# Performance work log

Measured on AMD Instinct MI355X. Metric: run time of the kernel, lower is better.

The kernel has to match this reference:

```python
import jax, jax.numpy as jnp
import numpy as np

KERNEL_SIZE = 4
STRIDE = 4


def setup_inputs() -> dict:
    key = jax.random.key(0)
    ks = jax.random.split(key, 5)
    b, l, d, hidden = 32, 8192, 256, 512
    x = jax.random.normal(ks[0], (b, l, d), dtype=jnp.float32)
    We = jax.random.normal(ks[1], (d, hidden), dtype=jnp.float32) * (1.0 / np.sqrt(d))
    be = jax.random.normal(ks[2], (hidden,), dtype=jnp.float32) * 0.01
    Wr = jax.random.normal(ks[3], (hidden, 1), dtype=jnp.float32) * (1.0 / np.sqrt(hidden))
    br = jax.random.normal(ks[4], (1,), dtype=jnp.float32) * 0.01
    return {"x": x, "We": We, "be": be, "Wr": Wr, "br": br}


def reference(x, We, be, Wr, br):
    b, l, d = x.shape
    steps = (l - KERNEL_SIZE) // STRIDE + 1
    # window gather: original loop slices x[:, i*stride : i*stride+stride, :]
    idx = jnp.arange(steps)[:, None] * STRIDE + jnp.arange(STRIDE)[None, :]  # (steps, stride)
    win = x[:, idx, :]  # (b, steps, stride, d)
    h = jnp.tanh(win @ We + be)                      # (b, steps, stride, hidden)
    logits = jnp.squeeze(h @ Wr, -1) + br            # (b, steps, stride)
    w = jax.nn.softmax(jax.nn.sigmoid(logits), axis=-1)
    out = jnp.einsum('bswd,bsw->bsd', win, w)        # softmax-weighted sum over window
    return out
```

## Files before the change

### kernel.cpp

```cpp
#include <hip/hip_runtime.h>
#include <hip/hip_bf16.h>

typedef __attribute__((ext_vector_type(8))) short bf16x8;
typedef __attribute__((ext_vector_type(4))) float f32x4;

#define D        256
#define NH       512
#define NT       32
#define KT       8
#define MT       4
#define ROWS_PER_BLOCK 64
#define ROWS_TOTAL (32*8192)
#define BFRAG    131072

typedef __attribute__((address_space(1))) const void GV;
typedef __attribute__((address_space(3))) void LV;

__device__ __forceinline__ short f2bf(float f) {
    union { float f; unsigned u; } v; v.f = f;
    unsigned r = v.u + 0x7FFFu + ((v.u >> 16) & 1u);
    return (short)(r >> 16);
}
__device__ __forceinline__ float rcp_fast(float x) {
    return __builtin_amdgcn_rcpf(x);
}

__global__ void prepack_B(const float* __restrict__ We, const float* __restrict__ be,
                          const float* __restrict__ Wr,
                          short* __restrict__ Bh, float2* __restrict__ bw,
                          float* __restrict__ Ssum, int ncopy) {
    int i = blockIdx.x * 256 + threadIdx.x;
    int k = i >> 9;
    int n = i & 511;
    int nt = n >> 4, c = n & 15;
    int kt = k >> 5, g = (k >> 3) & 3, j = k & 7;
    int idx = (((nt * 8 + kt) * 64) + (g * 16 + c)) * 8 + j;
    short v = f2bf(We[i]);
    for (int cp = 0; cp < ncopy; ++cp)
        Bh[cp * BFRAG + idx] = v;
    if (i < 512) bw[i] = make_float2(2.0f * be[i], Wr[i]);
    if (i == 0) {
        float s = 0.0f;
        for (int t = 0; t < 512; ++t) s += Wr[t];
        Ssum[0] = s;
    }
}

__global__ __launch_bounds__(64, 2) void softpool_main(
    const float* __restrict__ x, const short* __restrict__ Bh,
    const float2* __restrict__ bwg, const float* __restrict__ br,
    const float* __restrict__ Ssum, float* __restrict__ out, int cmask)
{
    const int lane = threadIdx.x;
    const int c = lane & 15;
    const int g = lane >> 4;
    const long row0 = (long)blockIdx.x * ROWS_PER_BLOCK;

    __shared__ short Bl[2][4096];
    __shared__ float2 bwl[512];

    const short* gB = Bh + (long)(blockIdx.x & cmask) * BFRAG + lane * 8;

    #define STAGE(buf, ntv) {                                                  \
        const short* _g = gB + (long)(ntv) * 4096;                             \
        _Pragma("unroll")                                                      \
        for (int kk = 0; kk < 8; ++kk)                                         \
            __builtin_amdgcn_global_load_lds((GV*)(_g + kk * 512),             \
                (LV*)&Bl[buf][kk * 512], 16, 0, 0);                            \
    }

    #define VM0 asm volatile("s_waitcnt vmcnt(0)" ::: "memory");

    STAGE(0, 0)

    #pragma unroll
    for (int i = 0; i < 4; ++i) {
        float4 v = ((const float4*)bwg)[lane * 4 + i];
        ((float4*)bwl)[lane * 4 + i] = v;
    }

    bf16x8 a[MT][KT];
    #pragma unroll
    for (int m = 0; m < MT; ++m) {
        const float* xr = x + (row0 + m * 16 + c) * D + g * 8;
        #pragma unroll
        for (int kt = 0; kt < KT; ++kt) {
            float4 v0 = *(const float4*)(xr + kt * 32);
            float4 v1 = *(const float4*)(xr + kt * 32 + 4);
            bf16x8 t;
            t[0] = f2bf(v0.x); t[1] = f2bf(v0.y); t[2] = f2bf(v0.z); t[3] = f2bf(v0.w);
            t[4] = f2bf(v1.x); t[5] = f2bf(v1.y); t[6] = f2bf(v1.z); t[7] = f2bf(v1.w);
            a[m][kt] = t;
        }
    }

    float lps[MT][4];
    #pragma unroll
    for (int m = 0; m < MT; ++m)
        #pragma unroll
        for (int r = 0; r < 4; ++r) lps[m][r] = 0.0f;

    f32x4 accA[MT], accB[MT];

    #define MFMA_(buf, accv) {                                                 \
        _Pragma("unroll")                                                      \
        for (int m = 0; m < MT; ++m)                                           \
            _Pragma("unroll")                                                  \
            for (int r = 0; r < 4; ++r) accv[m][r] = 0.0f;                     \
        _Pragma("unroll")                                                      \
        for (int kt = 0; kt < KT; ++kt) {                                      \
            bf16x8 b = *(const bf16x8*)&Bl[buf][kt * 512 + lane * 8];          \
            _Pragma("unroll")                                                  \
            for (int m = 0; m < MT; ++m)                                       \
                accv[m] = __builtin_amdgcn_mfma_f32_16x16x32_bf16(             \
                             a[m][kt], b, accv[m], 0, 0, 0);                   \
        }                                                                      \
    }

    #define TANH_(accv, ntv) {                                                 \
        float2 bwv = bwl[(ntv) * 16 + c];                                      \
        _Pragma("unroll")                                                      \
        for (int m = 0; m < MT; ++m)                                           \
            _Pragma("unroll")                                                  \
            for (int r = 0; r < 4; ++r) {                                      \
                float z = __builtin_fmaf(accv[m][r], 2.0f, bwv.x);             \
                float e = __expf(z);                                           \
                float rr = rcp_fast(e + 1.0f);                                 \
                lps[m][r] = __builtin_fmaf(bwv.y, rr, lps[m][r]);              \
            }                                                                  \
    }

    VM0
    STAGE(1, 1)
    MFMA_(0, accA)
    VM0

    for (int it = 0; it < 15; ++it) {
        STAGE(0, 2 * it + 2)
        MFMA_(1, accB)
        TANH_(accA, 2 * it)
        VM0
        STAGE(1, 2 * it + 3)
        MFMA_(0, accA)
        TANH_(accB, 2 * it + 1)
        VM0
    }
    MFMA_(1, accB)
    TANH_(accA, 30)
    TANH_(accB, 31)

    const float brv = br[0];
    const float S = Ssum[0];
    #pragma unroll
    for (int m = 0; m < MT; ++m) {
        float l0 = lps[m][0], l1 = lps[m][1], l2 = lps[m][2], l3 = lps[m][3];
        #pragma unroll
        for (int off = 1; off < 16; off <<= 1) {
            l0 += __shfl_xor(l0, off, 64);
            l1 += __shfl_xor(l1, off, 64);
            l2 += __shfl_xor(l2, off, 64);
            l3 += __shfl_xor(l3, off, 64);
        }
        float g0 = S - 2.0f * l0 + brv;
        float g1 = S - 2.0f * l1 + brv;
        float g2 = S - 2.0f * l2 + brv;
        float g3 = S - 2.0f * l3 + brv;
        float s0 = rcp_fast(1.0f + __expf(-g0));
        float s1 = rcp_fast(1.0f + __expf(-g1));
        float s2 = rcp_fast(1.0f + __expf(-g2));
        float s3 = rcp_fast(1.0f + __expf(-g3));
        float e0 = __expf(s0), e1 = __expf(s1), e2 = __expf(s2), e3 = __expf(s3);
        float inv = rcp_fast(e0 + e1 + e2 + e3);
        float w0 = e0 * inv, w1 = e1 * inv, w2 = e2 * inv, w3 = e3 * inv;

        const long wrow = row0 + m * 16 + g * 4;
        const long W = wrow >> 2;
        const float* xw = x + wrow * D + c * 4;
        float* op = out + W * D + c * 4;
        #pragma unroll
        for (int q = 0; q < 4; ++q) {
            float4 r0 = *(const float4*)(xw + 0 * D + q * 64);
            float4 r1 = *(const float4*)(xw + 1 * D + q * 64);
            float4 r2 = *(const float4*)(xw + 2 * D + q * 64);
            float4 r3 = *(const float4*)(xw + 3 * D + q * 64);
            float4 oo;
            oo.x = w0 * r0.x + w1 * r1.x + w2 * r2.x + w3 * r3.x;
            oo.y = w0 * r0.y + w1 * r1.y + w2 * r2.y + w3 * r3.y;
            oo.z = w0 * r0.z + w1 * r1.z + w2 * r2.z + w3 * r3.z;
            oo.w = w0 * r0.w + w1 * r1.w + w2 * r2.w + w3 * r3.w;
            *(float4*)(op + q * 64) = oo;
        }
    }
}

extern "C" void kernel_launch(void* const* d_in, const int* in_sizes, int n_in,
                              void* d_out, int out_size, void* d_ws, size_t ws_size,
                              hipStream_t stream) {
    const float* x  = (const float*)d_in[0];
    const float* We = (const float*)d_in[1];
    const float* be = (const float*)d_in[2];
    const float* Wr = (const float*)d_in[3];
    const float* br = (const float*)d_in[4];
    float* out = (float*)d_out;

    const int ncopy = (ws_size >= (size_t)8 * BFRAG * 2 + 8192) ? 8 : 1;

    char* ws = (char*)d_ws;
    short*  Bh   = (short*)ws;
    float2* bwp  = (float2*)(ws + (size_t)ncopy * BFRAG * 2);
    float*  Ssum = (float*)((char*)bwp + 4096);

    prepack_B<<<BFRAG / 256, 256, 0, stream>>>(We, be, Wr, Bh, bwp, Ssum, ncopy);

    const int blocks = ROWS_TOTAL / ROWS_PER_BLOCK;
    softpool_main<<<blocks, 64, 0, stream>>>(x, Bh, bwp, br, Ssum, out, ncopy - 1);
}
```

Measured before the change: 163.1 us.

## Load x rows coalesced and transpose through swizzled LDS; drop B replicas

The A-operand load now reads whole x rows with fully coalesced float4 loads, converts them to bf16, writes them into LDS with an XOR swizzle, and reads the MFMA fragments back from LDS. This replaces the earlier strided per-lane gathers. The LDS used is buffer 0 of the B double buffer, so B staging now starts in buffer 1 and the ping-pong order is swapped. The multiple replicated copies of the packed B weights are removed, so every block reads one shared copy. This shrinks the prepack work but may increase L2 contention on that single copy.

```diff
diff --git a/kernel.cpp b/kernel.cpp
--- a/kernel.cpp
+++ b/kernel.cpp
@@ -2,6 +2,7 @@
 #include <hip/hip_bf16.h>
 
 typedef __attribute__((ext_vector_type(8))) short bf16x8;
+typedef __attribute__((ext_vector_type(4))) short short4v;
 typedef __attribute__((ext_vector_type(4))) float f32x4;
 
 #define D        256
@@ -11,7 +12,6 @@
 #define MT       4
 #define ROWS_PER_BLOCK 64
 #define ROWS_TOTAL (32*8192)
-#define BFRAG    131072
 
 typedef __attribute__((address_space(1))) const void GV;
 typedef __attribute__((address_space(3))) void LV;
@@ -28,16 +28,14 @@
 __global__ void prepack_B(const float* __restrict__ We, const float* __restrict__ be,
                           const float* __restrict__ Wr,
                           short* __restrict__ Bh, float2* __restrict__ bw,
-                          float* __restrict__ Ssum, int ncopy) {
+                          float* __restrict__ Ssum) {
     int i = blockIdx.x * 256 + threadIdx.x;
     int k = i >> 9;
     int n = i & 511;
     int nt = n >> 4, c = n & 15;
     int kt = k >> 5, g = (k >> 3) & 3, j = k & 7;
     int idx = (((nt * 8 + kt) * 64) + (g * 16 + c)) * 8 + j;
-    short v = f2bf(We[i]);
-    for (int cp = 0; cp < ncopy; ++cp)
-        Bh[cp * BFRAG + idx] = v;
+    Bh[idx] = f2bf(We[i]);
     if (i < 512) bw[i] = make_float2(2.0f * be[i], Wr[i]);
     if (i == 0) {
         float s = 0.0f;
@@ -49,7 +47,7 @@
 __global__ __launch_bounds__(64, 2) void softpool_main(
     const float* __restrict__ x, const short* __restrict__ Bh,
     const float2* __restrict__ bwg, const float* __restrict__ br,
-    const float* __restrict__ Ssum, float* __restrict__ out, int cmask)
+    const float* __restrict__ Ssum, float* __restrict__ out)
 {
     const int lane = threadIdx.x;
     const int c = lane & 15;
@@ -59,7 +57,7 @@
     __shared__ short Bl[2][4096];
     __shared__ float2 bwl[512];
 
-    const short* gB = Bh + (long)(blockIdx.x & cmask) * BFRAG + lane * 8;
+    const short* gB = Bh + lane * 8;
 
     #define STAGE(buf, ntv) {                                                  \
         const short* _g = gB + (long)(ntv) * 4096;                             \
@@ -71,7 +69,7 @@
 
     #define VM0 asm volatile("s_waitcnt vmcnt(0)" ::: "memory");
 
-    STAGE(0, 0)
+    STAGE(1, 0)
 
     #pragma unroll
     for (int i = 0; i < 4; ++i) {
@@ -80,17 +78,30 @@
     }
 
     bf16x8 a[MT][KT];
+    char* Asl = (char*)&Bl[0][0];
     #pragma unroll
     for (int m = 0; m < MT; ++m) {
-        const float* xr = x + (row0 + m * 16 + c) * D + g * 8;
+        #pragma unroll
+        for (int half = 0; half < 2; ++half) {
+            const float* rb = x + (row0 + m * 16 + half * 8) * D;
+            float4 st[8];
+            #pragma unroll
+            for (int i = 0; i < 8; ++i)
+                st[i] = ((const float4*)(rb + i * D))[lane];
+            #pragma unroll
+            for (int i = 0; i < 8; ++i) {
+                const int row = half * 8 + i;
+                short4v t;
+                t[0] = f2bf(st[i].x); t[1] = f2bf(st[i].y);
+                t[2] = f2bf(st[i].z); t[3] = f2bf(st[i].w);
+                const int boff = row * 512 + ((lane * 8) ^ ((row & 7) << 4));
+                *(short4v*)(Asl + boff) = t;
+            }
+        }
         #pragma unroll
         for (int kt = 0; kt < KT; ++kt) {
-            float4 v0 = *(const float4*)(xr + kt * 32);
-            float4 v1 = *(const float4*)(xr + kt * 32 + 4);
-            bf16x8 t;
-            t[0] = f2bf(v0.x); t[1] = f2bf(v0.y); t[2] = f2bf(v0.z); t[3] = f2bf(v0.w);
-            t[4] = f2bf(v1.x); t[5] = f2bf(v1.y); t[6] = f2bf(v1.z); t[7] = f2bf(v1.w);
-            a[m][kt] = t;
+            const int boff = c * 512 + ((kt * 64 + g * 16) ^ ((c & 7) << 4));
+            a[m][kt] = *(const bf16x8*)(Asl + boff);
         }
     }
 
@@ -131,21 +142,21 @@
     }
 
     VM0
-    STAGE(1, 1)
-    MFMA_(0, accA)
+    STAGE(0, 1)
+    MFMA_(1, accA)
     VM0
 
     for (int it = 0; it < 15; ++it) {
-        STAGE(0, 2 * it + 2)
-        MFMA_(1, accB)
+        STAGE(1, 2 * it + 2)
+        MFMA_(0, accB)
         TANH_(accA, 2 * it)
         VM0
-        STAGE(1, 2 * it + 3)
-        MFMA_(0, accA)
+        STAGE(0, 2 * it + 3)
+        MFMA_(1, accA)
         TANH_(accB, 2 * it + 1)
         VM0
     }
-    MFMA_(1, accB)
+    MFMA_(0, accB)
     TANH_(accA, 30)
     TANH_(accB, 31)
 
@@ -203,15 +214,13 @@
     const float* br = (const float*)d_in[4];
     float* out = (float*)d_out;
 
-    const int ncopy = (ws_size >= (size_t)8 * BFRAG * 2 + 8192) ? 8 : 1;
-
     char* ws = (char*)d_ws;
     short*  Bh   = (short*)ws;
-    float2* bwp  = (float2*)(ws + (size_t)ncopy * BFRAG * 2);
-    float*  Ssum = (float*)((char*)bwp + 4096);
-
-    prepack_B<<<BFRAG / 256, 256, 0, stream>>>(We, be, Wr, Bh, bwp, Ssum, ncopy);
+    float2* bwp  = (float2*)(ws + 262144);
+    float*  Ssum = (float*)(ws + 262144 + 4096);
+
+    prepack_B<<<NH * D / 256, 256, 0, stream>>>(We, be, Wr, Bh, bwp, Ssum);
 
     const int blocks = ROWS_TOTAL / ROWS_PER_BLOCK;
-    softpool_main<<<blocks, 64, 0, stream>>>(x, Bh, bwp, br, Ssum, out, ncopy - 1);
-}
+    softpool_main<<<blocks, 64, 0, stream>>>(x, Bh, bwp, br, Ssum, out);
+}
```

Result: faster. 140.7 us (median of 2 runs) (-13.7%).
